# Kernel tuning notes

Measured on AMD Instinct MI355X. Metric: run time of the kernel, lower is better.

Reference implementation:

```python
import jax, jax.numpy as jnp
import numpy as np
import math

B, T, D, H = 2, 2048, 1024, 8
DK = D // H


def setup_inputs() -> dict:
    key = jax.random.key(0)
    ks = jax.random.split(key, 10)
    return {
        "query": jax.random.normal(ks[0], (B, T, D), jnp.float32),
        "key": jax.random.normal(ks[1], (B, T, D), jnp.float32),
        "value": jax.random.normal(ks[2], (B, T, D), jnp.float32),
        "mask": jnp.zeros((1, 1, T, T), dtype=bool),
        "rel_bias": jax.random.normal(ks[3], (B, T, T, H), jnp.float32) * 0.02,
        "Wq": jax.random.normal(ks[4], (D, D), jnp.float32) / math.sqrt(D),
        "Wk": jax.random.normal(ks[5], (D, D), jnp.float32) / math.sqrt(D),
        "Wv": jax.random.normal(ks[6], (D, D), jnp.float32) / math.sqrt(D),
        "Wo": jax.random.normal(ks[7], (D, D), jnp.float32) / math.sqrt(D),
        "bo": jnp.zeros((D,), jnp.float32),
        "is_causal": 1,
    }


def reference(query, key, value, mask, rel_bias, Wq, Wk, Wv, Wo, bo, is_causal):
    b, tq, d = query.shape
    # torch Linear: x @ W.T ; split into heads [B,H,T,DK]
    Q = (query @ Wq.T).reshape(b, tq, H, DK).transpose(0, 2, 1, 3)
    K = (key @ Wk.T).reshape(b, -1, H, DK).transpose(0, 2, 1, 3)
    V = (value @ Wv.T).reshape(b, -1, H, DK).transpose(0, 2, 1, 3)
    scores = jnp.einsum('bhqd,bhkd->bhqk', Q, K) / math.sqrt(DK)
    # rel_bias is [B,Tq,Tk,H] -> permute to [B,H,Tq,Tk]
    scores = scores + jnp.transpose(rel_bias, (0, 3, 1, 2))
    neg_inf = jnp.float32(-jnp.inf)
    scores = jnp.where(mask, neg_inf, scores)
    if is_causal:
        tk = scores.shape[-1]
        causal = jnp.triu(jnp.ones((tq, tk), dtype=bool), 1)
        scores = jnp.where(causal, neg_inf, scores)
    attn = jax.nn.softmax(scores, axis=-1)
    out = jnp.einsum('bhqk,bhkd->bhqd', attn, V)
    out = out.transpose(0, 2, 1, 3).reshape(b, tq, d)
    return out @ Wo.T + bo
```

## Files before the change

### kernel.cpp

```cpp
#include <hip/hip_runtime.h>
#include <stdint.h>
#include <stddef.h>

#define T_SEQ  2048
#define NBATCH 2
#define DMODEL 1024
#define NHEAD  8
#define DKH    128
#define MROWS  (NBATCH * T_SEQ)

typedef __attribute__((ext_vector_type(8))) short          short8;
typedef __attribute__((ext_vector_type(4))) float          f32x4;
typedef __attribute__((ext_vector_type(4))) unsigned short ushort4v;

__device__ __forceinline__ unsigned short f32_to_bf16(float f) {
    union { float f; uint32_t u; } v; v.f = f;
    uint32_t u = v.u;
    u += 0x7FFFu + ((u >> 16) & 1u);
    return (unsigned short)(u >> 16);
}

__device__ __forceinline__ f32x4 mfma_bf16(short8 a, short8 b, f32x4 c) {
    return __builtin_amdgcn_mfma_f32_16x16x32_bf16(a, b, c, 0, 0, 0);
}

__device__ __forceinline__ void gload_lds16(const unsigned short* g, unsigned short* l) {
    typedef __attribute__((address_space(1))) const unsigned int gas;
    typedef __attribute__((address_space(3))) unsigned int las;
    __builtin_amdgcn_global_load_lds((gas*)(uintptr_t)g, (las*)(uintptr_t)l, 16, 0, 0);
}

struct CvtDesc { const float* src; unsigned short* dst; int n4; };
struct CvtArgs { CvtDesc d[7]; };

__global__ void cvt_f32_to_bf16(CvtArgs args) {
    CvtDesc dd = args.d[blockIdx.y];
    typedef __attribute__((ext_vector_type(4))) float float4v;
    int stride = gridDim.x * blockDim.x;
    for (int i = blockIdx.x * blockDim.x + threadIdx.x; i < dd.n4; i += stride) {
        float4v v = ((const float4v*)dd.src)[i];
        ushort4v o;
        o.x = f32_to_bf16(v.x);
        o.y = f32_to_bf16(v.y);
        o.z = f32_to_bf16(v.z);
        o.w = f32_to_bf16(v.w);
        ((ushort4v*)dd.dst)[i] = o;
    }
}

template<int OUTMODE>
__device__ __forceinline__ void gemm_core(const unsigned short* __restrict__ A,
                                          const unsigned short* __restrict__ W,
                                          void* __restrict__ Cout,
                                          const float* __restrict__ bias)
{
    constexpr int N = DMODEL, K = DMODEL;
    __shared__ __align__(16) unsigned short As[128 * 32];
    __shared__ __align__(16) unsigned short Bs[128 * 32];

    const int tid  = threadIdx.x;
    const int w    = tid >> 6;
    const int lane = tid & 63;
    const int qr   = lane & 15;
    const int quad = lane >> 4;
    const int wm   = w >> 1;
    const int wn   = w & 1;
    const int bm   = blockIdx.y * 128;
    const int bn   = blockIdx.x * 128;

    const int srow = lane >> 2;
    const int sg   = lane & 3;

    f32x4 acc[4][4];
    #pragma unroll
    for (int i = 0; i < 4; ++i)
        #pragma unroll
        for (int j = 0; j < 4; ++j) {
            acc[i][j][0] = 0.f; acc[i][j][1] = 0.f;
            acc[i][j][2] = 0.f; acc[i][j][3] = 0.f;
        }

    for (int k0 = 0; k0 < K; k0 += 32) {
        __syncthreads();
        #pragma unroll
        for (int j = 0; j < 2; ++j) {
            const int row = w * 32 + j * 16 + srow;
            const int gg  = sg ^ ((row >> 2) & 3);
            gload_lds16(A + (size_t)(bm + row) * K + k0 + gg * 8,
                        &As[(w * 32 + j * 16) * 32]);
            gload_lds16(W + (size_t)(bn + row) * K + k0 + gg * 8,
                        &Bs[(w * 32 + j * 16) * 32]);
        }
        __syncthreads();

        short8 af[4], bf[4];
        #pragma unroll
        for (int mt = 0; mt < 4; ++mt) {
            const int row = wm * 64 + mt * 16 + qr;
            const int sl  = quad ^ ((row >> 2) & 3);
            af[mt] = *(const short8*)&As[row * 32 + sl * 8];
        }
        #pragma unroll
        for (int nt = 0; nt < 4; ++nt) {
            const int row = wn * 64 + nt * 16 + qr;
            const int sl  = quad ^ ((row >> 2) & 3);
            bf[nt] = *(const short8*)&Bs[row * 32 + sl * 8];
        }
        #pragma unroll
        for (int mt = 0; mt < 4; ++mt)
            #pragma unroll
            for (int nt = 0; nt < 4; ++nt)
                acc[mt][nt] = mfma_bf16(af[mt], bf[nt], acc[mt][nt]);
    }

    if (OUTMODE == 0) {
        unsigned short* C = (unsigned short*)Cout;
        #pragma unroll
        for (int mt = 0; mt < 4; ++mt)
            #pragma unroll
            for (int nt = 0; nt < 4; ++nt)
                #pragma unroll
                for (int r = 0; r < 4; ++r) {
                    const int row = bm + wm * 64 + mt * 16 + quad * 4 + r;
                    const int col = bn + wn * 64 + nt * 16 + qr;
                    C[(size_t)row * N + col] = f32_to_bf16(acc[mt][nt][r]);
                }
    } else {
        float* C = (float*)Cout;
        float bv[4];
        #pragma unroll
        for (int nt = 0; nt < 4; ++nt)
            bv[nt] = bias[bn + wn * 64 + nt * 16 + qr];
        #pragma unroll
        for (int mt = 0; mt < 4; ++mt)
            #pragma unroll
            for (int nt = 0; nt < 4; ++nt)
                #pragma unroll
                for (int r = 0; r < 4; ++r) {
                    const int row = bm + wm * 64 + mt * 16 + quad * 4 + r;
                    const int col = bn + wn * 64 + nt * 16 + qr;
                    C[(size_t)row * N + col] = acc[mt][nt][r] + bv[nt];
                }
    }
}

__global__ __launch_bounds__(256) void gemm_qkv(
    const unsigned short* Aq, const unsigned short* Ak, const unsigned short* Av,
    const unsigned short* Wq, const unsigned short* Wk, const unsigned short* Wv,
    unsigned short* Cq, unsigned short* Ck, unsigned short* Cv)
{
    const unsigned short* Ap[3] = {Aq, Ak, Av};
    const unsigned short* Wp[3] = {Wq, Wk, Wv};
    unsigned short*       Cp[3] = {Cq, Ck, Cv};
    const int z = blockIdx.z;
    gemm_core<0>(Ap[z], Wp[z], Cp[z], nullptr);
}

__global__ __launch_bounds__(256) void gemm_out(
    const unsigned short* A, const unsigned short* W, float* C, const float* bias)
{
    gemm_core<1>(A, W, C, bias);
}

__global__ void transpose_bf16(const unsigned short* __restrict__ src,
                               unsigned short* __restrict__ dst)
{
    __shared__ unsigned short t[32][33];
    const int x = threadIdx.x, y = threadIdx.y;
    const int c0 = blockIdx.x * 32, r0 = blockIdx.y * 32;
    t[y][x] = src[(size_t)(r0 + y) * DMODEL + c0 + x];
    __syncthreads();
    dst[(size_t)(c0 + y) * MROWS + r0 + x] = t[x][y];
}

__global__ __launch_bounds__(256) void flash_attn(
    const unsigned short* __restrict__ Qp,
    const unsigned short* __restrict__ Kp,
    const unsigned short* __restrict__ VT,
    const float* __restrict__ rel_bias,
    const int* __restrict__ is_causal,
    unsigned short* __restrict__ Oout)
{
    __shared__ __align__(16) unsigned short plds[4][16 * 40];

    const int tid  = threadIdx.x;
    const int w    = tid >> 6;
    const int lane = tid & 63;
    const int qr   = lane & 15;
    const int quad = lane >> 4;
    const int h    = blockIdx.z * 4 + w;
    const int q0   = blockIdx.x * 16;
    const int b    = blockIdx.y;
    const int causal = is_causal[0];
    const float scale = 0.08838834764831845f;

    short8 qf[4];
    {
        const size_t base = (size_t)(b * T_SEQ + q0 + qr) * DMODEL + h * DKH + quad * 8;
        #pragma unroll
        for (int ks = 0; ks < 4; ++ks)
            qf[ks] = *(const short8*)(Qp + base + ks * 32);
    }

    float m_i[4] = {-3.0e38f, -3.0e38f, -3.0e38f, -3.0e38f};
    float l_i[4] = {0.f, 0.f, 0.f, 0.f};
    f32x4 o[8];
    #pragma unroll
    for (int nd = 0; nd < 8; ++nd) {
        o[nd][0] = 0.f; o[nd][1] = 0.f; o[nd][2] = 0.f; o[nd][3] = 0.f;
    }

    const int kend = causal ? (q0 + 16) : T_SEQ;
    const float* biasBase = rel_bias
        + (size_t)(b * T_SEQ + q0 + quad * 4) * T_SEQ * NHEAD + h;

    for (int k0 = 0; k0 < kend; k0 += 32) {
        short8 kf[2][4];
        #pragma unroll
        for (int half = 0; half < 2; ++half) {
            const size_t rk = (size_t)(b * T_SEQ + k0 + half * 16 + qr) * DMODEL
                            + h * DKH + quad * 8;
            #pragma unroll
            for (int ks = 0; ks < 4; ++ks)
                kf[half][ks] = *(const short8*)(Kp + rk + ks * 32);
        }
        short8 vf[8];
        #pragma unroll
        for (int nd = 0; nd < 8; ++nd) {
            const size_t rv = (size_t)(h * DKH + nd * 16 + qr) * MROWS
                            + b * T_SEQ + k0 + quad * 8;
            vf[nd] = *(const short8*)(VT + rv);
        }

        f32x4 s[2];
        s[0][0]=0.f; s[0][1]=0.f; s[0][2]=0.f; s[0][3]=0.f;
        s[1][0]=0.f; s[1][1]=0.f; s[1][2]=0.f; s[1][3]=0.f;
        #pragma unroll
        for (int half = 0; half < 2; ++half)
            #pragma unroll
            for (int ks = 0; ks < 4; ++ks)
                s[half] = mfma_bf16(qf[ks], kf[half][ks], s[half]);

        float pv[2][4];
        #pragma unroll
        for (int r = 0; r < 4; ++r) {
            const int qg = q0 + quad * 4 + r;
            #pragma unroll
            for (int half = 0; half < 2; ++half) {
                const int kg = k0 + half * 16 + qr;
                const float bval = biasBase[(size_t)r * (T_SEQ * NHEAD)
                                            + (size_t)kg * NHEAD];
                float sv = s[half][r] * scale + bval;
                if (causal && (kg > qg)) sv = -3.0e38f;
                pv[half][r] = sv;
            }
        }

        #pragma unroll
        for (int r = 0; r < 4; ++r) {
            float tm = fmaxf(pv[0][r], pv[1][r]);
            #pragma unroll
            for (int d = 1; d < 16; d <<= 1) tm = fmaxf(tm, __shfl_xor(tm, d));
            const float mn = fmaxf(m_i[r], tm);
            const float alpha = __expf(m_i[r] - mn);
            m_i[r] = mn;
            const float p0 = __expf(pv[0][r] - mn);
            const float p1 = __expf(pv[1][r] - mn);
            pv[0][r] = p0; pv[1][r] = p1;
            float rs = p0 + p1;
            #pragma unroll
            for (int d = 1; d < 16; d <<= 1) rs += __shfl_xor(rs, d);
            l_i[r] = l_i[r] * alpha + rs;
            #pragma unroll
            for (int nd = 0; nd < 8; ++nd) o[nd][r] *= alpha;
        }

        unsigned short* pb = &plds[w][0];
        #pragma unroll
        for (int r = 0; r < 4; ++r) {
            pb[(quad * 4 + r) * 40 + qr]      = f32_to_bf16(pv[0][r]);
            pb[(quad * 4 + r) * 40 + 16 + qr] = f32_to_bf16(pv[1][r]);
        }
        const short8 pf = *(const short8*)&pb[qr * 40 + quad * 8];

        #pragma unroll
        for (int nd = 0; nd < 8; ++nd)
            o[nd] = mfma_bf16(pf, vf[nd], o[nd]);
    }

    float inv[4];
    #pragma unroll
    for (int r = 0; r < 4; ++r) inv[r] = 1.0f / l_i[r];
    #pragma unroll
    for (int nd = 0; nd < 8; ++nd)
        #pragma unroll
        for (int r = 0; r < 4; ++r) {
            const int qg = q0 + quad * 4 + r;
            Oout[(size_t)(b * T_SEQ + qg) * DMODEL + h * DKH + nd * 16 + qr]
                = f32_to_bf16(o[nd][r] * inv[r]);
        }
}

extern "C" void kernel_launch(void* const* d_in, const int* in_sizes, int n_in,
                              void* d_out, int out_size, void* d_ws, size_t ws_size,
                              hipStream_t stream)
{
    const float* query    = (const float*)d_in[0];
    const float* key      = (const float*)d_in[1];
    const float* value    = (const float*)d_in[2];
    const float* rel_bias = (const float*)d_in[4];
    const float* Wq       = (const float*)d_in[5];
    const float* Wk       = (const float*)d_in[6];
    const float* Wv       = (const float*)d_in[7];
    const float* Wo       = (const float*)d_in[8];
    const float* bo       = (const float*)d_in[9];
    const int*   is_causal= (const int*)d_in[10];

    char* ws = (char*)d_ws;
    const size_t SZ_X = (size_t)MROWS * DMODEL * 2;
    const size_t SZ_W = (size_t)DMODEL * DMODEL * 2;
    unsigned short* Xq  = (unsigned short*)(ws + 0 * SZ_X);
    unsigned short* Xk  = (unsigned short*)(ws + 1 * SZ_X);
    unsigned short* Xv  = (unsigned short*)(ws + 2 * SZ_X);
    unsigned short* Wqb = (unsigned short*)(ws + 3 * SZ_X);
    unsigned short* Wkb = (unsigned short*)(ws + 3 * SZ_X + 1 * SZ_W);
    unsigned short* Wvb = (unsigned short*)(ws + 3 * SZ_X + 2 * SZ_W);
    unsigned short* Wob = (unsigned short*)(ws + 3 * SZ_X + 3 * SZ_W);
    unsigned short* Qp  = (unsigned short*)(ws + 3 * SZ_X + 4 * SZ_W);
    unsigned short* Kp  = (unsigned short*)(ws + 4 * SZ_X + 4 * SZ_W);
    unsigned short* Vp  = (unsigned short*)(ws + 5 * SZ_X + 4 * SZ_W);
    unsigned short* VT  = Xk;
    unsigned short* AO  = Xq;

    CvtArgs ca;
    ca.d[0] = {query, Xq,  MROWS * DMODEL / 4};
    ca.d[1] = {key,   Xk,  MROWS * DMODEL / 4};
    ca.d[2] = {value, Xv,  MROWS * DMODEL / 4};
    ca.d[3] = {Wq,    Wqb, DMODEL * DMODEL / 4};
    ca.d[4] = {Wk,    Wkb, DMODEL * DMODEL / 4};
    ca.d[5] = {Wv,    Wvb, DMODEL * DMODEL / 4};
    ca.d[6] = {Wo,    Wob, DMODEL * DMODEL / 4};

    cvt_f32_to_bf16<<<dim3(1024, 7), dim3(256), 0, stream>>>(ca);

    gemm_qkv<<<dim3(DMODEL / 128, MROWS / 128, 3), dim3(256), 0, stream>>>(
        Xq, Xk, Xv, Wqb, Wkb, Wvb, Qp, Kp, Vp);

    transpose_bf16<<<dim3(DMODEL / 32, MROWS / 32), dim3(32, 32), 0, stream>>>(Vp, VT);

    flash_attn<<<dim3(T_SEQ / 16, NBATCH, NHEAD / 4), dim3(256), 0, stream>>>(
        Qp, Kp, VT, rel_bias, is_causal, AO);

    gemm_out<<<dim3(DMODEL / 128, MROWS / 128, 1), dim3(256), 0, stream>>>(
        AO, Wob, (float*)d_out, bo);
}
```

Before: 774.7 us.

## Pre-transpose relative bias to bf16 head-major and use 32-row attention tiles

Adds a kernel that converts rel_bias from [B,T,T,H] fp32 into a bf16 [B,H,T,T] buffer, skipping tiles fully masked by causality. A new attention kernel then reads contiguous bf16 bias per head and uses 2-wave blocks where each wave handles 32 query rows (two MFMA row tiles). Scores are staged through LDS to redistribute them across lanes. The aim is to cut the strided fp32 bias reads and raise K/V reuse per load, at the cost of an extra pass and a large workspace buffer. The old path is kept as a fallback when the workspace is too small.

```diff
diff --git a/kernel.cpp b/kernel.cpp
--- a/kernel.cpp
+++ b/kernel.cpp
@@ -18,6 +18,10 @@
     uint32_t u = v.u;
     u += 0x7FFFu + ((u >> 16) & 1u);
     return (unsigned short)(u >> 16);
+}
+__device__ __forceinline__ float bf16_to_f32(unsigned short s) {
+    union { uint32_t u; float f; } v; v.u = ((uint32_t)s) << 16;
+    return v.f;
 }
 
 __device__ __forceinline__ f32x4 mfma_bf16(short8 a, short8 b, f32x4 c) {
@@ -173,6 +177,190 @@
     dst[(size_t)(c0 + y) * MROWS + r0 + x] = t[x][y];
 }
 
+__global__ __launch_bounds__(256) void bias_transpose(
+    const float* __restrict__ src, unsigned short* __restrict__ dst,
+    const int* __restrict__ is_causal)
+{
+    const int k0 = blockIdx.x * 64;
+    const int q0 = blockIdx.y * 4;
+    const int b  = blockIdx.z;
+    if (is_causal[0] && k0 > q0 + 3) return;
+    const int q = q0 + (threadIdx.x >> 6);
+    const int k = k0 + (threadIdx.x & 63);
+
+    typedef __attribute__((ext_vector_type(4))) float float4v;
+    const float4v* s = (const float4v*)(src + (((size_t)(b * T_SEQ + q)) * T_SEQ + k) * NHEAD);
+    float4v v0 = s[0];
+    float4v v1 = s[1];
+    float hv[8] = {v0.x, v0.y, v0.z, v0.w, v1.x, v1.y, v1.z, v1.w};
+    #pragma unroll
+    for (int h = 0; h < NHEAD; ++h)
+        dst[((size_t)(b * NHEAD + h) * T_SEQ + q) * T_SEQ + k] = f32_to_bf16(hv[h]);
+}
+
+__global__ __launch_bounds__(128, 2) void flash_attn2(
+    const unsigned short* __restrict__ Qp,
+    const unsigned short* __restrict__ Kp,
+    const unsigned short* __restrict__ VT,
+    const unsigned short* __restrict__ biasT,
+    const int* __restrict__ is_causal,
+    unsigned short* __restrict__ Oout)
+{
+    __shared__ __align__(16) float Slds[2][32 * 36];
+
+    const int tid  = threadIdx.x;
+    const int w    = tid >> 6;
+    const int lane = tid & 63;
+    const int qr   = lane & 15;
+    const int quad = lane >> 4;
+    const int bh   = blockIdx.y;
+    const int b    = bh >> 3;
+    const int h    = bh & 7;
+    const int qbase = (blockIdx.x * 2 + w) * 32;
+    const int causal = is_causal[0];
+    const float scale = 0.08838834764831845f;
+    float* S = &Slds[w][0];
+
+    short8 qf[2][4];
+    #pragma unroll
+    for (int mt = 0; mt < 2; ++mt) {
+        const size_t base = (size_t)(b * T_SEQ + qbase + mt * 16 + qr) * DMODEL
+                          + h * DKH + quad * 8;
+        #pragma unroll
+        for (int ks = 0; ks < 4; ++ks)
+            qf[mt][ks] = *(const short8*)(Qp + base + ks * 32);
+    }
+
+    f32x4 o[2][8];
+    #pragma unroll
+    for (int mt = 0; mt < 2; ++mt)
+        #pragma unroll
+        for (int nd = 0; nd < 8; ++nd) {
+            o[mt][nd][0] = 0.f; o[mt][nd][1] = 0.f;
+            o[mt][nd][2] = 0.f; o[mt][nd][3] = 0.f;
+        }
+    float m_i[2] = {-3.0e38f, -3.0e38f};
+    float l_i[2] = {0.f, 0.f};
+
+    const int kend = causal ? (qbase + 32) : T_SEQ;
+
+    for (int k0 = 0; k0 < kend; k0 += 32) {
+        short8 kf[2][4];
+        #pragma unroll
+        for (int half = 0; half < 2; ++half) {
+            const size_t rk = (size_t)(b * T_SEQ + k0 + half * 16 + qr) * DMODEL
+                            + h * DKH + quad * 8;
+            #pragma unroll
+            for (int ks = 0; ks < 4; ++ks)
+                kf[half][ks] = *(const short8*)(Kp + rk + ks * 32);
+        }
+        short8 vf[8];
+        #pragma unroll
+        for (int nd = 0; nd < 8; ++nd) {
+            const size_t rv = (size_t)(h * DKH + nd * 16 + qr) * MROWS
+                            + b * T_SEQ + k0 + quad * 8;
+            vf[nd] = *(const short8*)(VT + rv);
+        }
+
+        f32x4 s[2][2];
+        #pragma unroll
+        for (int mt = 0; mt < 2; ++mt)
+            #pragma unroll
+            for (int half = 0; half < 2; ++half) {
+                s[mt][half][0] = 0.f; s[mt][half][1] = 0.f;
+                s[mt][half][2] = 0.f; s[mt][half][3] = 0.f;
+            }
+        #pragma unroll
+        for (int mt = 0; mt < 2; ++mt)
+            #pragma unroll
+            for (int half = 0; half < 2; ++half)
+                #pragma unroll
+                for (int ks = 0; ks < 4; ++ks)
+                    s[mt][half] = mfma_bf16(qf[mt][ks], kf[half][ks], s[mt][half]);
+
+        #pragma unroll
+        for (int mt = 0; mt < 2; ++mt)
+            #pragma unroll
+            for (int half = 0; half < 2; ++half)
+                #pragma unroll
+                for (int r = 0; r < 4; ++r)
+                    S[(mt * 16 + quad * 4 + r) * 36 + half * 16 + qr] = s[mt][half][r];
+
+        const bool need_mask = causal && (k0 + 32 > qbase);
+
+        #pragma unroll
+        for (int mt = 0; mt < 2; ++mt) {
+            f32x4 sa0 = *(const f32x4*)&S[(mt * 16 + qr) * 36 + quad * 8];
+            f32x4 sa1 = *(const f32x4*)&S[(mt * 16 + qr) * 36 + quad * 8 + 4];
+            float val[8] = {sa0[0], sa0[1], sa0[2], sa0[3],
+                            sa1[0], sa1[1], sa1[2], sa1[3]};
+
+            const short8 bb = *(const short8*)&biasT[
+                ((size_t)bh * T_SEQ + qbase + mt * 16 + qr) * T_SEQ + k0 + quad * 8];
+
+            const int qg = qbase + mt * 16 + qr;
+            #pragma unroll
+            for (int e = 0; e < 8; ++e) {
+                float sv = val[e] * scale + bf16_to_f32((unsigned short)bb[e]);
+                if (need_mask && (k0 + quad * 8 + e > qg)) sv = -3.0e38f;
+                val[e] = sv;
+            }
+
+            float tm = val[0];
+            #pragma unroll
+            for (int e = 1; e < 8; ++e) tm = fmaxf(tm, val[e]);
+            tm = fmaxf(tm, __shfl_xor(tm, 16));
+            tm = fmaxf(tm, __shfl_xor(tm, 32));
+
+            const float mn = fmaxf(m_i[mt], tm);
+            const float alpha = __expf(m_i[mt] - mn);
+            m_i[mt] = mn;
+
+            float rs = 0.f;
+            short8 pf;
+            #pragma unroll
+            for (int e = 0; e < 8; ++e) {
+                const float p = __expf(val[e] - mn);
+                rs += p;
+                pf[e] = (short)f32_to_bf16(p);
+            }
+            rs += __shfl_xor(rs, 16);
+            rs += __shfl_xor(rs, 32);
+            l_i[mt] = l_i[mt] * alpha + rs;
+
+            float alC[4];
+            #pragma unroll
+            for (int r = 0; r < 4; ++r)
+                alC[r] = __shfl(alpha, quad * 4 + r);
+            #pragma unroll
+            for (int nd = 0; nd < 8; ++nd)
+                #pragma unroll
+                for (int r = 0; r < 4; ++r)
+                    o[mt][nd][r] *= alC[r];
+
+            #pragma unroll
+            for (int nd = 0; nd < 8; ++nd)
+                o[mt][nd] = mfma_bf16(pf, vf[nd], o[mt][nd]);
+        }
+    }
+
+    #pragma unroll
+    for (int mt = 0; mt < 2; ++mt) {
+        float invC[4];
+        #pragma unroll
+        for (int r = 0; r < 4; ++r)
+            invC[r] = 1.0f / __shfl(l_i[mt], quad * 4 + r);
+        #pragma unroll
+        for (int nd = 0; nd < 8; ++nd)
+            #pragma unroll
+            for (int r = 0; r < 4; ++r) {
+                const int row = b * T_SEQ + qbase + mt * 16 + quad * 4 + r;
+                Oout[(size_t)row * DMODEL + h * DKH + nd * 16 + qr]
+                    = f32_to_bf16(o[mt][nd][r] * invC[r]);
+            }
+    }
+}
+
 __global__ __launch_bounds__(256) void flash_attn(
     const unsigned short* __restrict__ Qp,
     const unsigned short* __restrict__ Kp,
@@ -317,8 +505,9 @@
     const int*   is_causal= (const int*)d_in[10];
 
     char* ws = (char*)d_ws;
-    const size_t SZ_X = (size_t)MROWS * DMODEL * 2;
-    const size_t SZ_W = (size_t)DMODEL * DMODEL * 2;
+    const size_t SZ_X  = (size_t)MROWS * DMODEL * 2;
+    const size_t SZ_W  = (size_t)DMODEL * DMODEL * 2;
+    const size_t SZ_BT = (size_t)NBATCH * NHEAD * T_SEQ * T_SEQ * 2;
     unsigned short* Xq  = (unsigned short*)(ws + 0 * SZ_X);
     unsigned short* Xk  = (unsigned short*)(ws + 1 * SZ_X);
     unsigned short* Xv  = (unsigned short*)(ws + 2 * SZ_X);
@@ -329,8 +518,12 @@
     unsigned short* Qp  = (unsigned short*)(ws + 3 * SZ_X + 4 * SZ_W);
     unsigned short* Kp  = (unsigned short*)(ws + 4 * SZ_X + 4 * SZ_W);
     unsigned short* Vp  = (unsigned short*)(ws + 5 * SZ_X + 4 * SZ_W);
+    unsigned short* BT  = (unsigned short*)(ws + 6 * SZ_X + 4 * SZ_W);
     unsigned short* VT  = Xk;
     unsigned short* AO  = Xq;
+
+    const size_t need = 6 * SZ_X + 4 * SZ_W + SZ_BT;
+    const bool use_bt = (ws_size >= need);
 
     CvtArgs ca;
     ca.d[0] = {query, Xq,  MROWS * DMODEL / 4};
@@ -348,8 +541,15 @@
 
     transpose_bf16<<<dim3(DMODEL / 32, MROWS / 32), dim3(32, 32), 0, stream>>>(Vp, VT);
 
-    flash_attn<<<dim3(T_SEQ / 16, NBATCH, NHEAD / 4), dim3(256), 0, stream>>>(
-        Qp, Kp, VT, rel_bias, is_causal, AO);
+    if (use_bt) {
+        bias_transpose<<<dim3(T_SEQ / 64, T_SEQ / 4, NBATCH), dim3(256), 0, stream>>>(
+            rel_bias, BT, is_causal);
+        flash_attn2<<<dim3(T_SEQ / 64, NBATCH * NHEAD), dim3(128), 0, stream>>>(
+            Qp, Kp, VT, BT, is_causal, AO);
+    } else {
+        flash_attn<<<dim3(T_SEQ / 16, NBATCH, NHEAD / 4), dim3(256), 0, stream>>>(
+            Qp, Kp, VT, rel_bias, is_causal, AO);
+    }
 
     gemm_out<<<dim3(DMODEL / 128, MROWS / 128, 1), dim3(256), 0, stream>>>(
         AO, Wob, (float*)d_out, bo);
```

After: 652.8 us. 1.19x faster.
